# Kernel tuning notes

Measured on AMD Instinct MI355X. Metric: run time of the kernel, lower is better.

Reference implementation:

```python
import jax, jax.numpy as jnp
import numpy as np

D_IN = 1024
D_OUT = 1024
NUM_HEADS = 16
HEAD_DIM = D_OUT // NUM_HEADS


def setup_inputs() -> dict:
    key = jax.random.key(0)
    k_x, k_qkv, k_pw, k_pb = jax.random.split(key, 4)
    x = jax.random.normal(k_x, (2, 2048, D_IN), dtype=jnp.float32)
    # torch nn.Linear(d_in, 3*d_out, bias=False): weight [3*d_out, d_in]
    w_qkv = jax.random.normal(k_qkv, (3 * D_OUT, D_IN), dtype=jnp.float32) * (1.0 / np.sqrt(D_IN))
    # proj: nn.Linear(d_out, d_out) with bias
    w_proj = jax.random.normal(k_pw, (D_OUT, D_OUT), dtype=jnp.float32) * (1.0 / np.sqrt(D_OUT))
    b_proj = jax.random.normal(k_pb, (D_OUT,), dtype=jnp.float32) * 0.01
    return {"x": x, "w_qkv": w_qkv, "w_proj": w_proj, "b_proj": b_proj}


def reference(x, w_qkv, w_proj, b_proj):
    B, S, _ = x.shape
    # fused QKV projection: [B,S,3*D_OUT]
    qkv = jnp.einsum('bsd,ed->bse', x, w_qkv)
    qkv = qkv.reshape(B, S, 3, NUM_HEADS, HEAD_DIM)
    q, k, v = jnp.moveaxis(qkv, 2, 0)  # each [B,S,H,Dh]
    scale = 1.0 / jnp.sqrt(jnp.asarray(HEAD_DIM, dtype=x.dtype))
    # scores [B,H,S,S]
    scores = jnp.einsum('bqhd,bkhd->bhqk', q, k) * scale
    causal = jnp.tril(jnp.ones((S, S), dtype=bool))
    scores = jnp.where(causal, scores, jnp.asarray(-jnp.inf, dtype=scores.dtype))
    attn = jax.nn.softmax(scores, axis=-1)
    ctx = jnp.einsum('bhqk,bkhd->bqhd', attn, v)  # [B,S,H,Dh]
    ctx = ctx.reshape(B, S, D_OUT)
    return jnp.einsum('bsd,ed->bse', ctx, w_proj) + b_proj
```

## Files before the change

### kernel.cpp

```cpp
#include <hip/hip_runtime.h>
#include <hip/hip_bf16.h>
#include <cstdint>

#define B_SZ   2
#define S_LEN  2048
#define NH     16
#define LDA    72

using f32x4 = __attribute__((ext_vector_type(4))) float;
typedef __bf16 bf16x8 __attribute__((ext_vector_type(8)));
typedef __bf16 bf16x4 __attribute__((ext_vector_type(4)));

__device__ inline float bf2f(unsigned short u) {
    union { unsigned int i; float f; } v; v.i = ((unsigned int)u) << 16; return v.f;
}
__device__ inline unsigned short f2bf(float f) {
    union { float f; unsigned int i; } v; v.f = f;
    unsigned int r = v.i + 0x7fff + ((v.i >> 16) & 1);
    return (unsigned short)(r >> 16);
}
__device__ inline f32x4 mfma16(bf16x8 a, bf16x8 b, f32x4 c) {
    return __builtin_amdgcn_mfma_f32_16x16x32_bf16(a, b, c, 0, 0, 0);
}
__device__ inline void stC(float* C, size_t idx, float v)  { C[idx] = v; }
__device__ inline void stC(__bf16* C, size_t idx, float v) { ((unsigned short*)C)[idx] = f2bf(v); }

__global__ __launch_bounds__(256) void f2b2_kernel(
    const float* __restrict__ a, int na4, __bf16* __restrict__ outa,
    const float* __restrict__ b, int nb4, __bf16* __restrict__ outb)
{
    int i = blockIdx.x * blockDim.x + threadIdx.x;
    const float* src; __bf16* dst; int idx;
    if (i < na4)           { src = a; dst = outa; idx = i; }
    else if (i < na4 + nb4){ src = b; dst = outb; idx = i - na4; }
    else return;
    float4 v = ((const float4*)src)[idx];
    ushort4 o;
    o.x = f2bf(v.x); o.y = f2bf(v.y); o.z = f2bf(v.z); o.w = f2bf(v.w);
    ((ushort4*)dst)[idx] = o;
}

__global__ __launch_bounds__(256) void f2b_kernel(
    const float* __restrict__ in, __bf16* __restrict__ out, int n4)
{
    int i = blockIdx.x * blockDim.x + threadIdx.x;
    if (i < n4) {
        float4 v = ((const float4*)in)[i];
        ushort4 o;
        o.x = f2bf(v.x); o.y = f2bf(v.y); o.z = f2bf(v.z); o.w = f2bf(v.w);
        ((ushort4*)out)[i] = o;
    }
}

template <typename TO, int HAS_BIAS>
__global__ __launch_bounds__(256) void gemm128(
    const __bf16* __restrict__ A, const __bf16* __restrict__ W,
    const float* __restrict__ bias, TO* __restrict__ C,
    int M, int N, int K)
{
    __shared__ __bf16 Alds[2][128 * 32];
    __shared__ __bf16 Blds[2][128 * 32];
    const int tid  = threadIdx.x, lane = tid & 63, w = tid >> 6;
    const int c16  = lane & 15, quad = lane >> 4;
    const int mBase = blockIdx.y * 128, nBase = blockIdx.x * 128;
    const int moff = (w & 1) * 64, noff = (w >> 1) * 64;

    f32x4 acc[4][4];
#pragma unroll
    for (int i = 0; i < 4; ++i)
#pragma unroll
        for (int j = 0; j < 4; ++j) acc[i][j] = (f32x4){0.f, 0.f, 0.f, 0.f};

    auto stage = [&](int buf, int k0) {
#pragma unroll
        for (int p = 0; p < 2; ++p) {
            const int linear = p * 256 + tid;
            const int row = linear >> 2;
            const int seg = (linear & 3) ^ (row & 3);
            const int lbase = (p * 256 + w * 64) * 8;
            const __bf16* ga = A + (size_t)(mBase + row) * K + k0 + seg * 8;
            const __bf16* gb = W + (size_t)(nBase + row) * K + k0 + seg * 8;
            __builtin_amdgcn_global_load_lds(
                (const __attribute__((address_space(1))) void*)ga,
                (__attribute__((address_space(3))) void*)(&Alds[buf][lbase]), 16, 0, 0);
            __builtin_amdgcn_global_load_lds(
                (const __attribute__((address_space(1))) void*)gb,
                (__attribute__((address_space(3))) void*)(&Blds[buf][lbase]), 16, 0, 0);
        }
    };

    stage(0, 0);
    int cur = 0;
    for (int k0 = 0; k0 < K; k0 += 32) {
        __syncthreads();
        if (k0 + 32 < K) stage(cur ^ 1, k0 + 32);

        bf16x8 af[4], bw[4];
#pragma unroll
        for (int i = 0; i < 4; ++i) {
            const int rowA = moff + i * 16 + c16;
            af[i] = *(const bf16x8*)&Alds[cur][rowA * 32 + ((quad ^ (rowA & 3)) << 3)];
            const int rowB = noff + i * 16 + c16;
            bw[i] = *(const bf16x8*)&Blds[cur][rowB * 32 + ((quad ^ (rowB & 3)) << 3)];
        }
#pragma unroll
        for (int i = 0; i < 4; ++i)
#pragma unroll
            for (int j = 0; j < 4; ++j)
                acc[i][j] = mfma16(af[i], bw[j], acc[i][j]);
        cur ^= 1;
    }

#pragma unroll
    for (int j = 0; j < 4; ++j) {
        const int col = nBase + noff + j * 16 + c16;
        const float bv = HAS_BIAS ? bias[col] : 0.f;
#pragma unroll
        for (int i = 0; i < 4; ++i)
#pragma unroll
            for (int r = 0; r < 4; ++r) {
                const int row = mBase + moff + i * 16 + quad * 4 + r;
                stC(C, (size_t)row * N + col, acc[i][j][r] + bv);
            }
    }
}

__global__ __launch_bounds__(256) void attn(
    const __bf16* __restrict__ qkv, __bf16* __restrict__ ctx)
{
    __shared__ __bf16 Qs[64 * LDA];
    __shared__ __bf16 Ks[64 * LDA];
    __shared__ __bf16 Vs[64 * LDA];
    __shared__ __bf16 Ps[64 * LDA];

    const int tid  = threadIdx.x;
    const int lane = tid & 63;
    const int w    = tid >> 6;
    const int c16  = lane & 15;
    const int quad = lane >> 4;
    const int bh = blockIdx.x, b = bh >> 4, h = bh & 15;
    const int qt = (int)gridDim.y - 1 - (int)blockIdx.y;
    const int qBase = qt * 64;

    const float QS = 0.125f * 1.4426950408889634f;

    const int krow0 = tid >> 3;
    const int kd0   = (tid & 7) * 8;
    const int c16t = tid & 15;
    const int jh   = (tid >> 4) & 1;
    const int dblk = tid >> 5;

    const size_t rowB = (size_t)b * S_LEN;
    const __bf16* kp0 = qkv + (rowB + krow0) * 3072 + 1024 + h * 64 + kd0;
    const __bf16* kp1 = kp0 + (size_t)32 * 3072;
    const __bf16* vp0 = qkv + (rowB + 2 * jh * 16 + c16t) * 3072 + 2048 + h * 64 + dblk * 8;
    const __bf16* vp1 = vp0 + (size_t)16 * 3072;

    uint4 kr0 = *(const uint4*)kp0;
    uint4 kr1 = *(const uint4*)kp1;
    uint4 vr0 = *(const uint4*)vp0;
    uint4 vr1 = *(const uint4*)vp1;

#pragma unroll
    for (int p = 0; p < 2; ++p) {
        const int linear = p * 256 + tid;
        const int row = linear >> 3;
        const int d0 = (linear & 7) * 8;
        const __bf16* g = qkv + (rowB + qBase + row) * 3072 + h * 64 + d0;
        uint4 raw = *(const uint4*)g;
        const unsigned short* u = (const unsigned short*)&raw;
        unsigned short tmp[8];
#pragma unroll
        for (int jj = 0; jj < 8; ++jj) tmp[jj] = f2bf(bf2f(u[jj]) * QS);
        *(uint4*)&Qs[row * LDA + d0] = *(const uint4*)tmp;
    }
    __syncthreads();

    const bf16x8 aq0 = *(const bf16x8*)&Qs[(w * 16 + c16) * LDA + quad * 8];
    const bf16x8 aq1 = *(const bf16x8*)&Qs[(w * 16 + c16) * LDA + 32 + quad * 8];

    float l_r[4] = {0.f, 0.f, 0.f, 0.f};
    f32x4 acc_o[4];
#pragma unroll
    for (int j = 0; j < 4; ++j) acc_o[j] = (f32x4){0.f, 0.f, 0.f, 0.f};

    const int nCh = qt + 1;
    for (int cc = 0; cc < nCh; ++cc) {
        *(uint4*)&Ks[krow0 * LDA + kd0]        = kr0;
        *(uint4*)&Ks[(krow0 + 32) * LDA + kd0] = kr1;
        {
            const unsigned short* e1 = (const unsigned short*)&vr0;
            const unsigned short* e2 = (const unsigned short*)&vr1;
#pragma unroll
            for (int d = 0; d < 8; ++d) {
                const unsigned pack = (unsigned)e1[d] | ((unsigned)e2[d] << 16);
                *(unsigned*)&Vs[(dblk * 8 + d) * LDA + c16t * 4 + 2 * jh] = pack;
            }
        }
        __syncthreads();

        if (cc + 1 < nCh) {
            kp0 += (size_t)64 * 3072; kp1 += (size_t)64 * 3072;
            vp0 += (size_t)64 * 3072; vp1 += (size_t)64 * 3072;
            kr0 = *(const uint4*)kp0;
            kr1 = *(const uint4*)kp1;
            vr0 = *(const uint4*)vp0;
            vr1 = *(const uint4*)vp1;
        }

        f32x4 sc[4];
#pragma unroll
        for (int j = 0; j < 4; ++j) sc[j] = (f32x4){0.f, 0.f, 0.f, 0.f};
#pragma unroll
        for (int j = 0; j < 4; ++j) {
            bf16x8 bk0 = *(const bf16x8*)&Ks[(j * 16 + c16) * LDA + quad * 8];
            bf16x8 bk1 = *(const bf16x8*)&Ks[(j * 16 + c16) * LDA + 32 + quad * 8];
            sc[j] = mfma16(aq0, bk0, sc[j]);
            sc[j] = mfma16(aq1, bk1, sc[j]);
        }

        if (cc == nCh - 1) {
#pragma unroll
            for (int j = 0; j < 4; ++j) {
                const int key = cc * 64 + j * 16 + c16;
#pragma unroll
                for (int r = 0; r < 4; ++r) {
                    const int q = qBase + w * 16 + quad * 4 + r;
                    if (key > q) sc[j][r] = -1e30f;
                }
            }
        }

        float p_[4][4];
#pragma unroll
        for (int j = 0; j < 4; ++j)
#pragma unroll
            for (int r = 0; r < 4; ++r)
                p_[j][r] = exp2f(sc[j][r]);
#pragma unroll
        for (int r = 0; r < 4; ++r)
            l_r[r] += (p_[0][r] + p_[1][r]) + (p_[2][r] + p_[3][r]);

#pragma unroll
        for (int r = 0; r < 4; ++r) {
            bf16x4 pb;
            pb[0] = (__bf16)p_[0][r]; pb[1] = (__bf16)p_[1][r];
            pb[2] = (__bf16)p_[2][r]; pb[3] = (__bf16)p_[3][r];
            *(bf16x4*)&Ps[(w * 16 + quad * 4 + r) * LDA + c16 * 4] = pb;
        }

        bf16x8 ap0 = *(const bf16x8*)&Ps[(w * 16 + c16) * LDA + quad * 8];
        bf16x8 ap1 = *(const bf16x8*)&Ps[(w * 16 + c16) * LDA + 32 + quad * 8];
#pragma unroll
        for (int j = 0; j < 4; ++j) {
            bf16x8 bv0 = *(const bf16x8*)&Vs[(j * 16 + c16) * LDA + quad * 8];
            bf16x8 bv1 = *(const bf16x8*)&Vs[(j * 16 + c16) * LDA + 32 + quad * 8];
            acc_o[j] = mfma16(ap0, bv0, acc_o[j]);
            acc_o[j] = mfma16(ap1, bv1, acc_o[j]);
        }
        __syncthreads();
    }

#pragma unroll
    for (int r = 0; r < 4; ++r) {
        float l = l_r[r];
        l += __shfl_xor(l, 1);
        l += __shfl_xor(l, 2);
        l += __shfl_xor(l, 4);
        l += __shfl_xor(l, 8);
        const float inv = 1.0f / l;
        const size_t rowO = (rowB + qBase + w * 16 + quad * 4 + r) * 1024 + h * 64;
#pragma unroll
        for (int j = 0; j < 4; ++j)
            ctx[rowO + j * 16 + c16] = (__bf16)(acc_o[j][r] * inv);
    }
}

extern "C" void kernel_launch(void* const* d_in, const int* in_sizes, int n_in,
                              void* d_out, int out_size, void* d_ws, size_t ws_size,
                              hipStream_t stream) {
    const float* x      = (const float*)d_in[0];
    const float* w_qkv  = (const float*)d_in[1];
    const float* w_proj = (const float*)d_in[2];
    const float* b_proj = (const float*)d_in[3];
    float* out = (float*)d_out;

    __bf16* qkvb = (__bf16*)d_ws;
    __bf16* xb   = qkvb + (size_t)4096 * 3072;
    __bf16* wqb  = xb + (size_t)4096 * 1024;
    __bf16* ctxb = xb;
    __bf16* wpb  = wqb;

    const int M = B_SZ * S_LEN;
    const int nx4 = 4096 * 1024 / 4, nq4 = 3072 * 1024 / 4, np4 = 1024 * 1024 / 4;

    f2b2_kernel<<<(nx4 + nq4 + 255) / 256, 256, 0, stream>>>(x, nx4, xb, w_qkv, nq4, wqb);

    gemm128<__bf16, 0><<<dim3(3072 / 128, M / 128), 256, 0, stream>>>(
        xb, wqb, nullptr, qkvb, M, 3072, 1024);

    attn<<<dim3(B_SZ * NH, S_LEN / 64), 256, 0, stream>>>(qkvb, ctxb);

    f2b_kernel<<<(np4 + 255) / 256, 256, 0, stream>>>(w_proj, wpb, np4);

    gemm128<float, 1><<<dim3(1024 / 128, M / 128), 256, 0, stream>>>(
        ctxb, wpb, b_proj, out, M, 1024, 1024);
}
```

Baseline: 188.5 us.

## Pair causal query tiles per attention block and use 64-row tiles for output projection

The attention kernel now processes two query tiles per block, a long one (qt = NT-1-y) and a short one (qt = y), so every block gets roughly equal causal work and the grid is halved. The output projection switches to a new 64x128-tile GEMM, doubling its block count to fill more CUs on the small N=1024 problem. The w_proj conversion is also moved ahead of the attention launch. The cost is fewer attention blocks in flight and smaller GEMM tiles with less reuse per block.

```diff
diff --git a/kernel.cpp b/kernel.cpp
--- a/kernel.cpp
+++ b/kernel.cpp
@@ -5,6 +5,7 @@
 #define B_SZ   2
 #define S_LEN  2048
 #define NH     16
+#define NT     32
 #define LDA    72
 
 using f32x4 = __attribute__((ext_vector_type(4))) float;
@@ -125,21 +126,96 @@
     }
 }
 
-__global__ __launch_bounds__(256) void attn(
-    const __bf16* __restrict__ qkv, __bf16* __restrict__ ctx)
-{
-    __shared__ __bf16 Qs[64 * LDA];
-    __shared__ __bf16 Ks[64 * LDA];
-    __shared__ __bf16 Vs[64 * LDA];
-    __shared__ __bf16 Ps[64 * LDA];
-
-    const int tid  = threadIdx.x;
+template <typename TO, int HAS_BIAS>
+__global__ __launch_bounds__(256) void gemm64(
+    const __bf16* __restrict__ A, const __bf16* __restrict__ W,
+    const float* __restrict__ bias, TO* __restrict__ C,
+    int M, int N, int K)
+{
+    __shared__ __bf16 Alds[2][64 * 32];
+    __shared__ __bf16 Blds[2][128 * 32];
+    const int tid  = threadIdx.x, lane = tid & 63, w = tid >> 6;
+    const int c16  = lane & 15, quad = lane >> 4;
+    const int mBase = blockIdx.y * 64, nBase = blockIdx.x * 128;
+    const int moff = (w & 1) * 32, noff = (w >> 1) * 64;
+
+    f32x4 acc[2][4];
+#pragma unroll
+    for (int i = 0; i < 2; ++i)
+#pragma unroll
+        for (int j = 0; j < 4; ++j) acc[i][j] = (f32x4){0.f, 0.f, 0.f, 0.f};
+
+    auto stage = [&](int buf, int k0) {
+        {
+            const int row = tid >> 2;
+            const int seg = (tid & 3) ^ (row & 3);
+            const int lbase = (w * 64) * 8;
+            const __bf16* ga = A + (size_t)(mBase + row) * K + k0 + seg * 8;
+            __builtin_amdgcn_global_load_lds(
+                (const __attribute__((address_space(1))) void*)ga,
+                (__attribute__((address_space(3))) void*)(&Alds[buf][lbase]), 16, 0, 0);
+        }
+#pragma unroll
+        for (int p = 0; p < 2; ++p) {
+            const int linear = p * 256 + tid;
+            const int row = linear >> 2;
+            const int seg = (linear & 3) ^ (row & 3);
+            const int lbase = (p * 256 + w * 64) * 8;
+            const __bf16* gb = W + (size_t)(nBase + row) * K + k0 + seg * 8;
+            __builtin_amdgcn_global_load_lds(
+                (const __attribute__((address_space(1))) void*)gb,
+                (__attribute__((address_space(3))) void*)(&Blds[buf][lbase]), 16, 0, 0);
+        }
+    };
+
+    stage(0, 0);
+    int cur = 0;
+    for (int k0 = 0; k0 < K; k0 += 32) {
+        __syncthreads();
+        if (k0 + 32 < K) stage(cur ^ 1, k0 + 32);
+
+        bf16x8 af[2], bw[4];
+#pragma unroll
+        for (int i = 0; i < 2; ++i) {
+            const int rowA = moff + i * 16 + c16;
+            af[i] = *(const bf16x8*)&Alds[cur][rowA * 32 + ((quad ^ (rowA & 3)) << 3)];
+        }
+#pragma unroll
+        for (int j = 0; j < 4; ++j) {
+            const int rowB = noff + j * 16 + c16;
+            bw[j] = *(const bf16x8*)&Blds[cur][rowB * 32 + ((quad ^ (rowB & 3)) << 3)];
+        }
+#pragma unroll
+        for (int i = 0; i < 2; ++i)
+#pragma unroll
+            for (int j = 0; j < 4; ++j)
+                acc[i][j] = mfma16(af[i], bw[j], acc[i][j]);
+        cur ^= 1;
+    }
+
+#pragma unroll
+    for (int j = 0; j < 4; ++j) {
+        const int col = nBase + noff + j * 16 + c16;
+        const float bv = HAS_BIAS ? bias[col] : 0.f;
+#pragma unroll
+        for (int i = 0; i < 2; ++i)
+#pragma unroll
+            for (int r = 0; r < 4; ++r) {
+                const int row = mBase + moff + i * 16 + quad * 4 + r;
+                stC(C, (size_t)row * N + col, acc[i][j][r] + bv);
+            }
+    }
+}
+
+__device__ __forceinline__ void attn_tile(
+    const __bf16* __restrict__ qkv, __bf16* __restrict__ ctx,
+    int b, int h, int qt, int tid,
+    __bf16* Qs, __bf16* Ks, __bf16* Vs, __bf16* Ps)
+{
     const int lane = tid & 63;
     const int w    = tid >> 6;
     const int c16  = lane & 15;
     const int quad = lane >> 4;
-    const int bh = blockIdx.x, b = bh >> 4, h = bh & 15;
-    const int qt = (int)gridDim.y - 1 - (int)blockIdx.y;
     const int qBase = qt * 64;
 
     const float QS = 0.125f * 1.4426950408889634f;
@@ -276,6 +352,21 @@
     }
 }
 
+__global__ __launch_bounds__(256) void attn(
+    const __bf16* __restrict__ qkv, __bf16* __restrict__ ctx)
+{
+    __shared__ __bf16 Qs[64 * LDA];
+    __shared__ __bf16 Ks[64 * LDA];
+    __shared__ __bf16 Vs[64 * LDA];
+    __shared__ __bf16 Ps[64 * LDA];
+
+    const int bh = blockIdx.x, b = bh >> 4, h = bh & 15;
+    const int y  = blockIdx.y;
+
+    attn_tile(qkv, ctx, b, h, NT - 1 - y, threadIdx.x, Qs, Ks, Vs, Ps);
+    attn_tile(qkv, ctx, b, h, y,          threadIdx.x, Qs, Ks, Vs, Ps);
+}
+
 extern "C" void kernel_launch(void* const* d_in, const int* in_sizes, int n_in,
                               void* d_out, int out_size, void* d_ws, size_t ws_size,
                               hipStream_t stream) {
@@ -299,10 +390,10 @@
     gemm128<__bf16, 0><<<dim3(3072 / 128, M / 128), 256, 0, stream>>>(
         xb, wqb, nullptr, qkvb, M, 3072, 1024);
 
-    attn<<<dim3(B_SZ * NH, S_LEN / 64), 256, 0, stream>>>(qkvb, ctxb);
-
     f2b_kernel<<<(np4 + 255) / 256, 256, 0, stream>>>(w_proj, wpb, np4);
 
-    gemm128<float, 1><<<dim3(1024 / 128, M / 128), 256, 0, stream>>>(
+    attn<<<dim3(B_SZ * NH, NT / 2), 256, 0, stream>>>(qkvb, ctxb);
+
+    gemm64<float, 1><<<dim3(1024 / 128, M / 64), 256, 0, stream>>>(
         ctxb, wpb, b_proj, out, M, 1024, 1024);
 }
```

Result: no change. 190.9 us (+1.3%).
